# Optimization experiments

Measured on AMD Instinct MI355X. Metric: run time of the kernel, lower is better.

Reference implementation:

```python
import jax, jax.numpy as jnp
import numpy as np

N = 50000
DIM = 64
E = 800000


def setup_inputs() -> dict:
    key = jax.random.key(0)
    ks = jax.random.split(key, 12)
    s = 1.0 / np.sqrt(DIM)
    inp = {
        "x": jax.random.normal(ks[0], (N, DIM), dtype=jnp.float32),
        "coord": jax.random.normal(ks[1], (N, DIM), dtype=jnp.float32),
        "Wq": jax.random.uniform(ks[2], (DIM, DIM), jnp.float32, -s, s),
        "bq": jax.random.uniform(ks[3], (DIM,), jnp.float32, -s, s),
        "Wk": jax.random.uniform(ks[4], (DIM, DIM), jnp.float32, -s, s),
        "bk": jax.random.uniform(ks[5], (DIM,), jnp.float32, -s, s),
        "Wv": jax.random.uniform(ks[6], (DIM, DIM), jnp.float32, -s, s),
        "bv": jax.random.uniform(ks[7], (DIM,), jnp.float32, -s, s),
        "Wc": jax.random.uniform(ks[8], (DIM, 1), jnp.float32, -1.0, 1.0),
        "bc": jax.random.uniform(ks[9], (DIM,), jnp.float32, -1.0, 1.0),
        "edge_index": jax.random.randint(ks[10], (2, E), 0, N, dtype=jnp.int64),
    }
    return inp


def reference(x, coord, Wq, bq, Wk, bk, Wv, bv, Wc, bc, edge_index):
    row, col = edge_index[0], edge_index[1]
    # per-edge coordinate differences and distances: [E, DIM], [E, 1]
    dx = coord[row] - coord[col]
    dist = jnp.linalg.norm(dx, axis=-1, keepdims=True)
    # per-edge QKV projections (torch Linear: x @ W.T + b): [E, DIM]
    q = x[row] @ Wq.T + bq
    k = x[col] @ Wk.T + bk
    v = x[col] @ Wv.T + bv
    # scalar attention logit per edge, GLOBAL softmax over all edges (dim=0)
    attn = jnp.sum(q * k, axis=-1, keepdims=True)  # [E, 1]
    weight = jax.nn.softmax(attn, axis=0)          # [E, 1]
    delta_x = weight * v                            # [E, DIM]
    delta_coord = weight * (dist @ Wc.T + bc) * dx  # [E, DIM]
    # scatter-add back to nodes
    x_out = jax.ops.segment_sum(delta_x, row, num_segments=x.shape[0])
    coord_out = jax.ops.segment_sum(delta_coord, row, num_segments=coord.shape[0])
    return (x + x_out, coord + coord_out)
```

## Files before the change

kernel.cpp:

```cpp
#include <hip/hip_runtime.h>
#include <math.h>

#define N_NODES 50000
#define DIM 64
#define NE 800000
#define NSCAN_BLOCKS ((N_NODES + 255) / 256)
#define NGROUPS 8
#define ROWS_PER_GROUP ((N_NODES + NGROUPS - 1) / NGROUPS)
#define NFILL_GRID (392 * NGROUPS)

static __device__ __forceinline__ float bf2f(unsigned short u) {
    return __uint_as_float(((unsigned int)u) << 16);
}
static __device__ __forceinline__ unsigned short f2bf(float f) {
    unsigned int u = __float_as_uint(f);
    u += 0x7fffu + ((u >> 16) & 1u);
    return (unsigned short)(u >> 16);
}

typedef float v2f __attribute__((ext_vector_type(2)));
template <bool HI>
static __device__ __forceinline__ v2f fp8x2(unsigned int u) {
    return __builtin_amdgcn_cvt_pk_f32_fp8((int)u, HI);
}
static __device__ __forceinline__ unsigned int pack4_fp8(float a, float b,
                                                         float c, float d) {
    int p = __builtin_amdgcn_cvt_pk_fp8_f32(a, b, 0, false);
    p = __builtin_amdgcn_cvt_pk_fp8_f32(c, d, p, true);
    return (unsigned int)p;
}


__global__ __launch_bounds__(256, 5) void k_qkv(
    const float* __restrict__ x, const float* __restrict__ coord,
    const float* __restrict__ Wq, const float* __restrict__ bq,
    const float* __restrict__ Wk, const float* __restrict__ bk,
    const float* __restrict__ Wv, const float* __restrict__ bv,
    float* __restrict__ Qf, unsigned short* __restrict__ KVC)
{
    __shared__ ushort4 WT2[3][1024];
    __shared__ float4  xs4[32][16];

    const int tid  = threadIdx.x;
    const int base = blockIdx.x * 32;
    unsigned int* U32 = (unsigned int*)KVC;

    for (int t = tid; t < 1024; t += 256) {
        int d = t & 63, j2 = t >> 6;
        float4 a = ((const float4*)Wq)[d * 16 + j2];
        float4 b = ((const float4*)Wk)[d * 16 + j2];
        float4 c = ((const float4*)Wv)[d * 16 + j2];
        WT2[0][t] = make_ushort4(f2bf(a.x), f2bf(a.y), f2bf(a.z), f2bf(a.w));
        WT2[1][t] = make_ushort4(f2bf(b.x), f2bf(b.y), f2bf(b.z), f2bf(b.w));
        WT2[2][t] = make_ushort4(f2bf(c.x), f2bf(c.y), f2bf(c.z), f2bf(c.w));
    }
    for (int t = tid; t < 512; t += 256) {
        int n = base + (t >> 4), j = t & 15;
        if (n < N_NODES) {
            float4 cv = ((const float4*)coord)[(size_t)n * 16 + j];
            U32[(size_t)n * 64 + 48 + j] = pack4_fp8(cv.x, cv.y, cv.z, cv.w);
        }
    }
    for (int t = tid; t < 512; t += 256) {
        int r = t >> 4, j2 = t & 15;
        if (base + r < N_NODES)
            xs4[r][j2] = ((const float4*)x)[(size_t)(base + r) * 16 + j2];
    }
    __syncthreads();

    const int wv = tid >> 6;
    const int d  = tid & 63;
    const float bqv = bq[d], bkv = bk[d], bvv = bv[d];

    float aq[8], ak[8], av[8];
    #pragma unroll
    for (int r = 0; r < 8; ++r) { aq[r] = bqv; ak[r] = bkv; av[r] = bvv; }

    #pragma unroll 4
    for (int j2 = 0; j2 < 16; ++j2) {
        ushort4 uq = WT2[0][j2 * 64 + d];
        ushort4 uk = WT2[1][j2 * 64 + d];
        ushort4 uv = WT2[2][j2 * 64 + d];
        float wqx = bf2f(uq.x), wqy = bf2f(uq.y), wqz = bf2f(uq.z), wqw = bf2f(uq.w);
        float wkx = bf2f(uk.x), wky = bf2f(uk.y), wkz = bf2f(uk.z), wkw = bf2f(uk.w);
        float wvx = bf2f(uv.x), wvy = bf2f(uv.y), wvz = bf2f(uv.z), wvw = bf2f(uv.w);
        #pragma unroll
        for (int r = 0; r < 8; ++r) {
            float4 xv = xs4[wv * 8 + r][j2];
            aq[r] += xv.x * wqx + xv.y * wqy + xv.z * wqz + xv.w * wqw;
            ak[r] += xv.x * wkx + xv.y * wky + xv.z * wkz + xv.w * wkw;
            av[r] += xv.x * wvx + xv.y * wvy + xv.z * wvz + xv.w * wvw;
        }
    }
    #pragma unroll
    for (int r = 0; r < 8; ++r) {
        int n = base + wv * 8 + r;
        if (n < N_NODES) {
            Qf[(size_t)n * DIM + d] = aq[r];
            KVC[(size_t)n * 128 + d] = f2bf(ak[r]);
        }
    }
    __syncthreads();
    float* vf = (float*)xs4;
    #pragma unroll
    for (int r = 0; r < 8; ++r)
        vf[(wv * 8 + r) * 64 + d] = av[r];
    __syncthreads();
    for (int t = tid; t < 512; t += 256) {
        int ln = t >> 4, j = t & 15;
        int n = base + ln;
        if (n < N_NODES) {
            float4 vv = ((const float4*)vf)[ln * 16 + j];
            U32[(size_t)n * 64 + 32 + j] = pack4_fp8(vv.x, vv.y, vv.z, vv.w);
        }
    }
}

__global__ __launch_bounds__(256) void k_hist(
    const int* __restrict__ eidx, int* __restrict__ counts)
{
    const int grp = blockIdx.x & (NGROUPS - 1);
    const int blk = blockIdx.x >> 3;
    const int nblk = gridDim.x >> 3;
    const int rlo = grp * ROWS_PER_GROUP;
    const int rhi = rlo + ROWS_PER_GROUP;
    for (int e = blk * 256 + threadIdx.x; e < NE; e += nblk * 256) {
        int r = eidx[e];
        if (r >= rlo && r < rhi) atomicAdd(counts + r, 1);
    }
}

__global__ __launch_bounds__(256) void k_scan1(
    const int* __restrict__ counts, int* __restrict__ offsets,
    int* __restrict__ bsums)
{
    __shared__ int tmp[256];
    int i = blockIdx.x * 256 + threadIdx.x;
    int v = (i < N_NODES) ? counts[i] : 0;
    tmp[threadIdx.x] = v;
    __syncthreads();
    #pragma unroll
    for (int off = 1; off < 256; off <<= 1) {
        int t = (threadIdx.x >= off) ? tmp[threadIdx.x - off] : 0;
        __syncthreads();
        tmp[threadIdx.x] += t;
        __syncthreads();
    }
    if (i < N_NODES) offsets[i] = tmp[threadIdx.x] - v;
    if (threadIdx.x == 255) bsums[blockIdx.x] = tmp[255];
}

__global__ __launch_bounds__(256) void k_scan23(
    int* __restrict__ offsets, int* __restrict__ counts,
    const int* __restrict__ bsums)
{
    __shared__ int red[4];
    const int tid = threadIdx.x;
    const int b   = blockIdx.x;
    int v = (tid < b && tid < NSCAN_BLOCKS) ? bsums[tid] : 0;
    #pragma unroll
    for (int off = 32; off; off >>= 1) v += __shfl_xor(v, off);
    if ((tid & 63) == 0) red[tid >> 6] = v;
    __syncthreads();
    const int pre = red[0] + red[1] + red[2] + red[3];

    int i = b * 256 + tid;
    if (i < N_NODES) {
        int o = offsets[i] + pre;
        offsets[i] = o;
        counts[i]  = o;
    }
    if (i == 0) offsets[N_NODES] = NE;
}

__global__ __launch_bounds__(256) void k_fill(
    const int* __restrict__ eidx, int* __restrict__ cursor,
    int* __restrict__ bucket_col)
{
    const int grp = blockIdx.x & (NGROUPS - 1);
    const int blk = blockIdx.x >> 3;
    const int nblk = gridDim.x >> 3;
    const int rlo = grp * ROWS_PER_GROUP;
    const int rhi = rlo + ROWS_PER_GROUP;
    const int* __restrict__ cols = eidx + NE;
    for (int e = blk * 256 + threadIdx.x; e < NE; e += nblk * 256) {
        int r = eidx[e];
        if (r >= rlo && r < rhi) {
            int pos = atomicAdd(cursor + r, 1);
            bucket_col[pos] = cols[e];
        }
    }
}

__global__ __launch_bounds__(256) void k_edge_fused(
    const int* __restrict__ bucket_col, const int* __restrict__ offsets,
    const float* __restrict__ Qf, const unsigned short* __restrict__ KVC,
    const float* __restrict__ coord,
    const float* __restrict__ Wc, const float* __restrict__ bc,
    float* __restrict__ out_x, float* __restrict__ out_c,
    float* __restrict__ wsum)
{
    const int lane = threadIdx.x & 63;
    const int n = (blockIdx.x * 256 + threadIdx.x) >> 6;
    if (n >= N_NODES) return;
    const int qt = lane >> 4;
    const int sl = lane & 15;

    const float4 q4  = ((const float4*)Qf)[(size_t)n * 16 + sl];
    const float4 cr4 = ((const float4*)coord)[(size_t)n * 16 + sl];
    const float4 wc4 = ((const float4*)Wc)[sl];
    const float4 bc4 = ((const float4*)bc)[sl];
    const ushort4* K16 = (const ushort4*)KVC;
    const unsigned int* U32 = (const unsigned int*)KVC;

    const int s = offsets[n], t = offsets[n + 1];
    float4 accx = {0.f, 0.f, 0.f, 0.f};
    float4 accc = {0.f, 0.f, 0.f, 0.f};
    float psum = 0.0f;

    for (int base = s; base < t; base += 8) {
        int pos0 = base + qt;
        int pos1 = base + 4 + qt;
        bool v0 = pos0 < t, v1 = pos1 < t;
        int c0 = bucket_col[v0 ? pos0 : (t - 1)];
        int c1 = bucket_col[v1 ? pos1 : (t - 1)];
        ushort4      ku0 = K16[(size_t)c0 * 32 + sl];
        unsigned int vu0 = U32[(size_t)c0 * 64 + 32 + sl];
        unsigned int cu0 = U32[(size_t)c0 * 64 + 48 + sl];
        ushort4      ku1 = K16[(size_t)c1 * 32 + sl];
        unsigned int vu1 = U32[(size_t)c1 * 64 + 32 + sl];
        unsigned int cu1 = U32[(size_t)c1 * 64 + 48 + sl];

        v2f c0a = fp8x2<false>(cu0), c0b = fp8x2<true>(cu0);
        v2f c1a = fp8x2<false>(cu1), c1b = fp8x2<true>(cu1);

        float d0 = q4.x * bf2f(ku0.x) + q4.y * bf2f(ku0.y)
                 + q4.z * bf2f(ku0.z) + q4.w * bf2f(ku0.w);
        float dx0x = cr4.x - c0a.x, dx0y = cr4.y - c0a.y;
        float dx0z = cr4.z - c0b.x, dx0w = cr4.w - c0b.y;
        float e0 = dx0x * dx0x + dx0y * dx0y + dx0z * dx0z + dx0w * dx0w;
        float d1 = q4.x * bf2f(ku1.x) + q4.y * bf2f(ku1.y)
                 + q4.z * bf2f(ku1.z) + q4.w * bf2f(ku1.w);
        float dx1x = cr4.x - c1a.x, dx1y = cr4.y - c1a.y;
        float dx1z = cr4.z - c1b.x, dx1w = cr4.w - c1b.y;
        float e1 = dx1x * dx1x + dx1y * dx1y + dx1z * dx1z + dx1w * dx1w;

        #pragma unroll
        for (int off = 1; off <= 8; off <<= 1) {
            d0 += __shfl_xor(d0, off);
            e0 += __shfl_xor(e0, off);
            d1 += __shfl_xor(d1, off);
            e1 += __shfl_xor(e1, off);
        }
        float p0e = v0 ? __expf(d0) : 0.0f;
        float p1e = v1 ? __expf(d1) : 0.0f;
        float dist0 = sqrtf(e0), dist1 = sqrtf(e1);
        psum += p0e + p1e;

        v2f v0a = fp8x2<false>(vu0), v0b = fp8x2<true>(vu0);
        v2f v1a = fp8x2<false>(vu1), v1b = fp8x2<true>(vu1);
        accx.x += p0e * v0a.x + p1e * v1a.x;
        accx.y += p0e * v0a.y + p1e * v1a.y;
        accx.z += p0e * v0b.x + p1e * v1b.x;
        accx.w += p0e * v0b.y + p1e * v1b.y;
        accc.x += p0e * (dist0 * wc4.x + bc4.x) * dx0x
                + p1e * (dist1 * wc4.x + bc4.x) * dx1x;
        accc.y += p0e * (dist0 * wc4.y + bc4.y) * dx0y
                + p1e * (dist1 * wc4.y + bc4.y) * dx1y;
        accc.z += p0e * (dist0 * wc4.z + bc4.z) * dx0z
                + p1e * (dist1 * wc4.z + bc4.z) * dx1z;
        accc.w += p0e * (dist0 * wc4.w + bc4.w) * dx0w
                + p1e * (dist1 * wc4.w + bc4.w) * dx1w;
    }

    #pragma unroll
    for (int off = 16; off <= 32; off <<= 1) {
        accx.x += __shfl_xor(accx.x, off);
        accx.y += __shfl_xor(accx.y, off);
        accx.z += __shfl_xor(accx.z, off);
        accx.w += __shfl_xor(accx.w, off);
        accc.x += __shfl_xor(accc.x, off);
        accc.y += __shfl_xor(accc.y, off);
        accc.z += __shfl_xor(accc.z, off);
        accc.w += __shfl_xor(accc.w, off);
        psum   += __shfl_xor(psum, off);
    }
    if (lane < 16) {
        ((float4*)out_x)[(size_t)n * 16 + sl] = accx;
        ((float4*)out_c)[(size_t)n * 16 + sl] = accc;
    }
    if (lane == 0) wsum[n] = psum;
}

__global__ __launch_bounds__(1024) void k_redsum(
    const float* __restrict__ wsum, float* __restrict__ S)
{
    __shared__ float red[16];
    float a = 0.0f;
    for (int i = threadIdx.x; i < N_NODES; i += 1024) a += wsum[i];
    #pragma unroll
    for (int off = 32; off; off >>= 1) a += __shfl_xor(a, off);
    if ((threadIdx.x & 63) == 0) red[threadIdx.x >> 6] = a;
    __syncthreads();
    if (threadIdx.x == 0) {
        float s = 0.0f;
        #pragma unroll
        for (int w = 0; w < 16; ++w) s += red[w];
        *S = s;
    }
}

__global__ __launch_bounds__(256) void k_finalize(
    const float* __restrict__ x, const float* __restrict__ coord,
    const float* __restrict__ S, float* __restrict__ out)
{
    const float inv = 1.0f / *S;
    const int nd4 = (N_NODES * DIM) / 4;
    const float4* x4 = (const float4*)x;
    const float4* c4 = (const float4*)coord;
    float4* o4 = (float4*)out;
    for (int i = blockIdx.x * 256 + threadIdx.x; i < 2 * nd4;
         i += gridDim.x * 256) {
        float4 r = (i < nd4) ? x4[i] : c4[i - nd4];
        float4 a = o4[i];
        a.x = r.x + a.x * inv;
        a.y = r.y + a.y * inv;
        a.z = r.z + a.z * inv;
        a.w = r.w + a.w * inv;
        o4[i] = a;
    }
}

extern "C" void kernel_launch(void* const* d_in, const int* in_sizes, int n_in,
                              void* d_out, int out_size, void* d_ws, size_t ws_size,
                              hipStream_t stream)
{
    const float* x     = (const float*)d_in[0];
    const float* coord = (const float*)d_in[1];
    const float* Wq    = (const float*)d_in[2];
    const float* bq    = (const float*)d_in[3];
    const float* Wk    = (const float*)d_in[4];
    const float* bk    = (const float*)d_in[5];
    const float* Wv    = (const float*)d_in[6];
    const float* bv    = (const float*)d_in[7];
    const float* Wc    = (const float*)d_in[8];
    const float* bc    = (const float*)d_in[9];
    const int*   eidx  = (const int*)d_in[10];

    float* out = (float*)d_out;
    float* ws  = (float*)d_ws;

    float* Qf = ws;
    unsigned short* KVC = (unsigned short*)(Qf + (size_t)N_NODES * DIM);
    int* bucket_col = (int*)(KVC + (size_t)N_NODES * 128);
    int* counts  = bucket_col + NE;
    int* offsets = counts + N_NODES;
    int* bsums   = offsets + N_NODES + 1;
    float* wsum  = (float*)(bsums + 256);
    float* S     = wsum + N_NODES;

    float* out_x = out;
    float* out_c = out + (size_t)N_NODES * DIM;

    (void)hipMemsetAsync(counts, 0, (size_t)N_NODES * sizeof(int), stream);
    k_hist  <<<NFILL_GRID, 256, 0, stream>>>(eidx, counts);
    k_scan1 <<<NSCAN_BLOCKS, 256, 0, stream>>>(counts, offsets, bsums);
    k_scan23<<<NSCAN_BLOCKS, 256, 0, stream>>>(offsets, counts, bsums);
    k_fill  <<<NFILL_GRID, 256, 0, stream>>>(eidx, counts, bucket_col);

    k_qkv<<<(N_NODES + 31) / 32, 256, 0, stream>>>(
        x, coord, Wq, bq, Wk, bk, Wv, bv, Qf, KVC);

    k_edge_fused<<<(N_NODES * 64 + 255) / 256, 256, 0, stream>>>(
        bucket_col, offsets, Qf, KVC, coord, Wc, bc, out_x, out_c, wsum);

    k_redsum<<<1, 1024, 0, stream>>>(wsum, S);
    k_finalize<<<2048, 256, 0, stream>>>(x, coord, S, out);
}
```

Baseline: 201.6 us.

## Store Q/K as fp16 with fdot2, interleave V and coord fp8, exp2

Q and K are now stored as fp16. Q is pre-scaled by log2(e), so the edge kernel computes logits with packed fp16 dot2 instructions and uses exp2f instead of expf. V and coord fp8 values are packed into a single uint2 per lane, so each edge needs one 8-byte gather instead of two 4-byte gathers. Q storage shrinks from fp32 to fp16, which cuts gather bytes and ALU work per edge. Finalize now uses one thread per float4 with a full-size grid instead of a grid-stride loop; the fp16 range for Q and K is a precision risk.

```diff
diff --git a/kernel.cpp b/kernel.cpp
--- a/kernel.cpp
+++ b/kernel.cpp
@@ -9,16 +9,41 @@
 #define ROWS_PER_GROUP ((N_NODES + NGROUPS - 1) / NGROUPS)
 #define NFILL_GRID (392 * NGROUPS)
 
-static __device__ __forceinline__ float bf2f(unsigned short u) {
-    return __uint_as_float(((unsigned int)u) << 16);
-}
 static __device__ __forceinline__ unsigned short f2bf(float f) {
     unsigned int u = __float_as_uint(f);
     u += 0x7fffu + ((u >> 16) & 1u);
     return (unsigned short)(u >> 16);
 }
-
+static __device__ __forceinline__ float bf2f(unsigned short u) {
+    return __uint_as_float(((unsigned int)u) << 16);
+}
+
+typedef _Float16 half2v __attribute__((ext_vector_type(2)));
 typedef float v2f __attribute__((ext_vector_type(2)));
+
+static __device__ __forceinline__ half2v u2h(unsigned int u) {
+    union { unsigned int u; half2v h; } x; x.u = u; return x.h;
+}
+static __device__ __forceinline__ unsigned short f2h(float f) {
+    union { _Float16 h; unsigned short s; } x; x.h = (_Float16)f; return x.s;
+}
+
+#if defined(__has_builtin)
+#  if __has_builtin(__builtin_amdgcn_fdot2)
+#    define HAVE_FDOT2 1
+#  endif
+#endif
+
+static __device__ __forceinline__ float dot2acc(unsigned int qa,
+                                                unsigned int ka, float c) {
+#ifdef HAVE_FDOT2
+    return __builtin_amdgcn_fdot2(u2h(qa), u2h(ka), c, false);
+#else
+    half2v q = u2h(qa), k = u2h(ka);
+    return c + (float)q.x * (float)k.x + (float)q.y * (float)k.y;
+#endif
+}
+
 template <bool HI>
 static __device__ __forceinline__ v2f fp8x2(unsigned int u) {
     return __builtin_amdgcn_cvt_pk_f32_fp8((int)u, HI);
@@ -36,14 +61,13 @@
     const float* __restrict__ Wq, const float* __restrict__ bq,
     const float* __restrict__ Wk, const float* __restrict__ bk,
     const float* __restrict__ Wv, const float* __restrict__ bv,
-    float* __restrict__ Qf, unsigned short* __restrict__ KVC)
+    unsigned short* __restrict__ Qh, unsigned short* __restrict__ KVC)
 {
     __shared__ ushort4 WT2[3][1024];
     __shared__ float4  xs4[32][16];
 
     const int tid  = threadIdx.x;
     const int base = blockIdx.x * 32;
-    unsigned int* U32 = (unsigned int*)KVC;
 
     for (int t = tid; t < 1024; t += 256) {
         int d = t & 63, j2 = t >> 6;
@@ -53,13 +77,6 @@
         WT2[0][t] = make_ushort4(f2bf(a.x), f2bf(a.y), f2bf(a.z), f2bf(a.w));
         WT2[1][t] = make_ushort4(f2bf(b.x), f2bf(b.y), f2bf(b.z), f2bf(b.w));
         WT2[2][t] = make_ushort4(f2bf(c.x), f2bf(c.y), f2bf(c.z), f2bf(c.w));
-    }
-    for (int t = tid; t < 512; t += 256) {
-        int n = base + (t >> 4), j = t & 15;
-        if (n < N_NODES) {
-            float4 cv = ((const float4*)coord)[(size_t)n * 16 + j];
-            U32[(size_t)n * 64 + 48 + j] = pack4_fp8(cv.x, cv.y, cv.z, cv.w);
-        }
     }
     for (int t = tid; t < 512; t += 256) {
         int r = t >> 4, j2 = t & 15;
@@ -96,8 +113,8 @@
     for (int r = 0; r < 8; ++r) {
         int n = base + wv * 8 + r;
         if (n < N_NODES) {
-            Qf[(size_t)n * DIM + d] = aq[r];
-            KVC[(size_t)n * 128 + d] = f2bf(ak[r]);
+            Qh[(size_t)n * 64 + d]  = f2h(aq[r] * 1.44269504f);
+            KVC[(size_t)n * 128 + d] = f2h(ak[r]);
         }
     }
     __syncthreads();
@@ -106,12 +123,17 @@
     for (int r = 0; r < 8; ++r)
         vf[(wv * 8 + r) * 64 + d] = av[r];
     __syncthreads();
+    uint2* VC2 = (uint2*)KVC;
     for (int t = tid; t < 512; t += 256) {
         int ln = t >> 4, j = t & 15;
         int n = base + ln;
         if (n < N_NODES) {
             float4 vv = ((const float4*)vf)[ln * 16 + j];
-            U32[(size_t)n * 64 + 32 + j] = pack4_fp8(vv.x, vv.y, vv.z, vv.w);
+            float4 cv = ((const float4*)coord)[(size_t)n * 16 + j];
+            uint2 o;
+            o.x = pack4_fp8(vv.x, vv.y, vv.z, vv.w);
+            o.y = pack4_fp8(cv.x, cv.y, cv.z, cv.w);
+            VC2[(size_t)n * 32 + 16 + j] = o;
         }
     }
 }
@@ -194,7 +216,7 @@
 
 __global__ __launch_bounds__(256) void k_edge_fused(
     const int* __restrict__ bucket_col, const int* __restrict__ offsets,
-    const float* __restrict__ Qf, const unsigned short* __restrict__ KVC,
+    const unsigned short* __restrict__ Qh, const unsigned short* __restrict__ KVC,
     const float* __restrict__ coord,
     const float* __restrict__ Wc, const float* __restrict__ bc,
     float* __restrict__ out_x, float* __restrict__ out_c,
@@ -206,12 +228,12 @@
     const int qt = lane >> 4;
     const int sl = lane & 15;
 
-    const float4 q4  = ((const float4*)Qf)[(size_t)n * 16 + sl];
+    const uint2 q2   = ((const uint2*)Qh)[(size_t)n * 16 + sl];
     const float4 cr4 = ((const float4*)coord)[(size_t)n * 16 + sl];
     const float4 wc4 = ((const float4*)Wc)[sl];
     const float4 bc4 = ((const float4*)bc)[sl];
-    const ushort4* K16 = (const ushort4*)KVC;
-    const unsigned int* U32 = (const unsigned int*)KVC;
+    const uint2* K2  = (const uint2*)KVC;
+    const uint2* VC2 = (const uint2*)KVC;
 
     const int s = offsets[n], t = offsets[n + 1];
     float4 accx = {0.f, 0.f, 0.f, 0.f};
@@ -224,23 +246,20 @@
         bool v0 = pos0 < t, v1 = pos1 < t;
         int c0 = bucket_col[v0 ? pos0 : (t - 1)];
         int c1 = bucket_col[v1 ? pos1 : (t - 1)];
-        ushort4      ku0 = K16[(size_t)c0 * 32 + sl];
-        unsigned int vu0 = U32[(size_t)c0 * 64 + 32 + sl];
-        unsigned int cu0 = U32[(size_t)c0 * 64 + 48 + sl];
-        ushort4      ku1 = K16[(size_t)c1 * 32 + sl];
-        unsigned int vu1 = U32[(size_t)c1 * 64 + 32 + sl];
-        unsigned int cu1 = U32[(size_t)c1 * 64 + 48 + sl];
-
-        v2f c0a = fp8x2<false>(cu0), c0b = fp8x2<true>(cu0);
-        v2f c1a = fp8x2<false>(cu1), c1b = fp8x2<true>(cu1);
-
-        float d0 = q4.x * bf2f(ku0.x) + q4.y * bf2f(ku0.y)
-                 + q4.z * bf2f(ku0.z) + q4.w * bf2f(ku0.w);
+        uint2 k0  = K2[(size_t)c0 * 32 + sl];
+        uint2 vc0 = VC2[(size_t)c0 * 32 + 16 + sl];
+        uint2 k1  = K2[(size_t)c1 * 32 + sl];
+        uint2 vc1 = VC2[(size_t)c1 * 32 + 16 + sl];
+
+        v2f c0a = fp8x2<false>(vc0.y), c0b = fp8x2<true>(vc0.y);
+        v2f c1a = fp8x2<false>(vc1.y), c1b = fp8x2<true>(vc1.y);
+
+        float d0 = dot2acc(q2.y, k0.y, dot2acc(q2.x, k0.x, 0.0f));
+        float d1 = dot2acc(q2.y, k1.y, dot2acc(q2.x, k1.x, 0.0f));
+
         float dx0x = cr4.x - c0a.x, dx0y = cr4.y - c0a.y;
         float dx0z = cr4.z - c0b.x, dx0w = cr4.w - c0b.y;
         float e0 = dx0x * dx0x + dx0y * dx0y + dx0z * dx0z + dx0w * dx0w;
-        float d1 = q4.x * bf2f(ku1.x) + q4.y * bf2f(ku1.y)
-                 + q4.z * bf2f(ku1.z) + q4.w * bf2f(ku1.w);
         float dx1x = cr4.x - c1a.x, dx1y = cr4.y - c1a.y;
         float dx1z = cr4.z - c1b.x, dx1w = cr4.w - c1b.y;
         float e1 = dx1x * dx1x + dx1y * dx1y + dx1z * dx1z + dx1w * dx1w;
@@ -252,13 +271,13 @@
             d1 += __shfl_xor(d1, off);
             e1 += __shfl_xor(e1, off);
         }
-        float p0e = v0 ? __expf(d0) : 0.0f;
-        float p1e = v1 ? __expf(d1) : 0.0f;
+        float p0e = v0 ? exp2f(d0) : 0.0f;
+        float p1e = v1 ? exp2f(d1) : 0.0f;
         float dist0 = sqrtf(e0), dist1 = sqrtf(e1);
         psum += p0e + p1e;
 
-        v2f v0a = fp8x2<false>(vu0), v0b = fp8x2<true>(vu0);
-        v2f v1a = fp8x2<false>(vu1), v1b = fp8x2<true>(vu1);
+        v2f v0a = fp8x2<false>(vc0.x), v0b = fp8x2<true>(vc0.x);
+        v2f v1a = fp8x2<false>(vc1.x), v1b = fp8x2<true>(vc1.x);
         accx.x += p0e * v0a.x + p1e * v1a.x;
         accx.y += p0e * v0a.y + p1e * v1a.y;
         accx.z += p0e * v0b.x + p1e * v1b.x;
@@ -319,8 +338,8 @@
     const float4* x4 = (const float4*)x;
     const float4* c4 = (const float4*)coord;
     float4* o4 = (float4*)out;
-    for (int i = blockIdx.x * 256 + threadIdx.x; i < 2 * nd4;
-         i += gridDim.x * 256) {
+    int i = blockIdx.x * 256 + threadIdx.x;
+    if (i < 2 * nd4) {
         float4 r = (i < nd4) ? x4[i] : c4[i - nd4];
         float4 a = o4[i];
         a.x = r.x + a.x * inv;
@@ -350,8 +369,8 @@
     float* out = (float*)d_out;
     float* ws  = (float*)d_ws;
 
-    float* Qf = ws;
-    unsigned short* KVC = (unsigned short*)(Qf + (size_t)N_NODES * DIM);
+    unsigned short* Qh  = (unsigned short*)ws;
+    unsigned short* KVC = Qh + (size_t)N_NODES * 64;
     int* bucket_col = (int*)(KVC + (size_t)N_NODES * 128);
     int* counts  = bucket_col + NE;
     int* offsets = counts + N_NODES;
@@ -369,11 +388,12 @@
     k_fill  <<<NFILL_GRID, 256, 0, stream>>>(eidx, counts, bucket_col);
 
     k_qkv<<<(N_NODES + 31) / 32, 256, 0, stream>>>(
-        x, coord, Wq, bq, Wk, bk, Wv, bv, Qf, KVC);
+        x, coord, Wq, bq, Wk, bk, Wv, bv, Qh, KVC);
 
     k_edge_fused<<<(N_NODES * 64 + 255) / 256, 256, 0, stream>>>(
-        bucket_col, offsets, Qf, KVC, coord, Wc, bc, out_x, out_c, wsum);
+        bucket_col, offsets, Qh, KVC, coord, Wc, bc, out_x, out_c, wsum);
 
     k_redsum<<<1, 1024, 0, stream>>>(wsum, S);
-    k_finalize<<<2048, 256, 0, stream>>>(x, coord, S, out);
-}
+    k_finalize<<<(2 * N_NODES * DIM / 4 + 255) / 256, 256, 0, stream>>>(
+        x, coord, S, out);
+}
```

Measured after the change: 198.6 us (median of 2 runs). About the same (-1.5%).
